# Kernel tuning notes

Hardware: AMD Instinct MI355X
Metric: run time of the kernel (lower is better)

## Reference

```python
import jax, jax.numpy as jnp
import numpy as np

D_MODEL = 512
H = 8
C = 2


def setup_inputs() -> dict:
    key = jax.random.key(0)
    kq, kk, kv = jax.random.split(key, 3)
    B, L = 16, 1024
    Q = jax.random.normal(kq, (B, L, D_MODEL), dtype=jnp.float32)
    K = jax.random.normal(kk, (B, L, D_MODEL), dtype=jnp.float32)
    V = jax.random.normal(kv, (B, L, D_MODEL), dtype=jnp.float32)
    return {"Q": Q, "K": K, "V": V}


def reference(Q, K, V):
    B, L, dm = Q.shape
    d = dm // H
    # [B, h, L, d]
    q = Q.reshape(B, L, H, d).transpose(0, 2, 1, 3)
    k = K.reshape(B, L, H, d).transpose(0, 2, 1, 3)
    v = V.reshape(B, L, H, d).transpose(0, 2, 1, 3)

    # auto-correlation via FFT along the time axis (axis=2)
    qf = jnp.fft.fft(q, axis=2)
    kf = jnp.fft.fft(k, axis=2)
    corr = jnp.fft.ifft(qf * jnp.conj(kf), axis=2).real.astype(Q.dtype)  # [B,h,L,d]

    topk = int(C * np.log(L))  # static
    # top-k over the lag axis (L); lax.top_k works on last axis
    w, idx = jax.lax.top_k(corr.transpose(0, 1, 3, 2), topk)  # [B,h,d,k]
    w = jax.nn.softmax(w, axis=-1)
    w = w.transpose(0, 1, 3, 2)      # [B,h,k,d]
    idx = idx.transpose(0, 1, 3, 2)  # [B,h,k,d]

    # time-delay aggregation: out[t] = sum_i w_i * v[min(idx_i + t, L-1)]
    t = jnp.arange(L)
    gidx = jnp.minimum(idx[:, :, :, None, :] + t[None, None, None, :, None], L - 1)  # [B,h,k,L,d]
    gathered = jnp.take_along_axis(v[:, :, None, :, :], gidx, axis=3)  # [B,h,k,L,d]
    out = jnp.einsum('bhkd,bhkld->bhld', w, gathered)  # [B,h,L,d]

    return out.transpose(0, 2, 1, 3).reshape(B, L, dm)
```

## Files before the change

kernel.cpp:

```cpp
#include <hip/hip_runtime.h>
#include <float.h>

#define LSEQ 1024
#define NCH  8192
#define TOPK 13

typedef short bf16x8 __attribute__((ext_vector_type(8)));
typedef float f32x16 __attribute__((ext_vector_type(16)));

#define CH_BYTES 12416

__device__ __forceinline__ unsigned swzA(unsigned a) {
  return a ^ ((a >> 3) & 48u) ^ ((a >> 1) & 32u);
}
__device__ __forceinline__ float resid(float x) {
  return x - __uint_as_float(__float_as_uint(x) & 0xffff0000u);
}
__device__ __forceinline__ f32x16 mfma_bf16(bf16x8 a, bf16x8 b, f32x16 c) {
  return __builtin_amdgcn_mfma_f32_32x32x16_bf16(a, b, c, 0, 0, 0);
}

__global__ __launch_bounds__(256) void corr_mega_kernel(const float* __restrict__ Qg,
                                                        const float* __restrict__ Kg,
                                                        const float* __restrict__ Vg,
                                                        float* __restrict__ outg) {
  __shared__ __align__(16) unsigned char lds_raw[4 * CH_BYTES];
  const int tid = threadIdx.x, wave = tid >> 6, lane = tid & 63;
  const int bid = blockIdx.x;
  const int cblk = (bid & 7) * 256 + (bid >> 3);
  const int cg0 = cblk * 4;
  const int b = cg0 >> 9, col0 = cg0 & 511;
  const int c = cg0 + wave;
  (void)c;
  unsigned char* myc = lds_raw + wave * CH_BYTES;

  {
    const float* Qb = Qg + ((size_t)b * 1024) * 512 + col0;
    const float* Kb = Kg + ((size_t)b * 1024) * 512 + col0;
#pragma unroll
    for (int j = 0; j < 4; ++j) {
      int t = tid + 256 * j;
      float4 kv = *(const float4*)(Kb + (size_t)t * 512);
      float4 qv = *(const float4*)(Qb + (size_t)t * 512);
      unsigned ka0 = swzA(4u * (unsigned)(t >> 1) + 2u * (unsigned)(t & 1));
      unsigned qa0 = 8u * (unsigned)(t >> 1) + 2u * (unsigned)(t & 1);
      float karr[4] = {kv.x, kv.y, kv.z, kv.w};
      float qarr[4] = {qv.x, qv.y, qv.z, qv.w};
#pragma unroll
      for (int cc = 0; cc < 4; ++cc) {
        unsigned char* ck = lds_raw + cc * CH_BYTES;
        unsigned khiv = __float_as_uint(karr[cc]) >> 16;
        unsigned klov = __float_as_uint(resid(karr[cc])) >> 16;
        *(unsigned short*)(ck + ka0)        = (unsigned short)khiv;
        *(unsigned short*)(ck + 2048 + ka0) = (unsigned short)klov;
        unsigned qhiv = __float_as_uint(qarr[cc]) >> 16;
        unsigned qlov = __float_as_uint(resid(qarr[cc])) >> 16;
        *(unsigned short*)(ck + 4096 + qa0)     = (unsigned short)qhiv;
        *(unsigned short*)(ck + 4096 + qa0 + 4) = (unsigned short)qlov;
        if (t < 8) {
          *(unsigned short*)(ck + 8192 + qa0)     = (unsigned short)qhiv;
          *(unsigned short*)(ck + 8192 + qa0 + 4) = (unsigned short)qlov;
        }
      }
    }
  }
  __syncthreads();

  {
    unsigned* qe = (unsigned*)(myc + 4096);
    unsigned* qo = (unsigned*)(myc + 8256);
    uint4 r0 = *(const uint4*)(qe + 16 * lane);
    uint4 r1 = *(const uint4*)(qe + 16 * lane + 4);
    uint4 r2 = *(const uint4*)(qe + 16 * lane + 8);
    uint4 r3 = *(const uint4*)(qe + 16 * lane + 12);
    uint2 r4 = *(const uint2*)(qe + 16 * lane + 16);
    unsigned h9[9] = {r0.x, r0.z, r1.x, r1.z, r2.x, r2.z, r3.x, r3.z, r4.x};
    unsigned l9[9] = {r0.y, r0.w, r1.y, r1.w, r2.y, r2.w, r3.y, r3.w, r4.y};
    unsigned o16[16];
#pragma unroll
    for (int i = 0; i < 8; ++i) {
      o16[2 * i]     = __builtin_amdgcn_alignbyte(h9[i + 1], h9[i], 2);
      o16[2 * i + 1] = __builtin_amdgcn_alignbyte(l9[i + 1], l9[i], 2);
    }
    *(uint4*)(qo + 16 * lane)      = make_uint4(o16[0],  o16[1],  o16[2],  o16[3]);
    *(uint4*)(qo + 16 * lane + 4)  = make_uint4(o16[4],  o16[5],  o16[6],  o16[7]);
    *(uint4*)(qo + 16 * lane + 8)  = make_uint4(o16[8],  o16[9],  o16[10], o16[11]);
    *(uint4*)(qo + 16 * lane + 12) = make_uint4(o16[12], o16[13], o16[14], o16[15]);
    if (lane == 0) {
      *(uint4*)(qo + 1024) = make_uint4(o16[0], o16[1], o16[2], o16[3]);
      *(uint4*)(qo + 1028) = make_uint4(o16[4], o16[5], o16[6], o16[7]);
    }
  }

  const int row = lane & 31, Hh = lane >> 5;
  const int rp  = 2 * (row & 15) + (row >> 4);
  unsigned e0   = (unsigned)((8 * Hh - rp) & 1023);
  const int par = rp & 1;
  const unsigned char* bArr = myc + (par ? 8256 : 4096);
  unsigned boff = (((par ? (e0 - 1) : e0) >> 1) * 8u);
  unsigned tb   = (unsigned)(64 * row + 16 * Hh);

  f32x16 d = {};
#pragma unroll 4
  for (int ks = 0; ks < 64; ++ks) {
    unsigned sa = swzA(tb);
    uint4 Ah = *(const uint4*)(myc + sa);
    uint4 Al = *(const uint4*)(myc + 2048 + sa);
    uint2 p0 = *(const uint2*)(bArr + boff);
    uint2 p1 = *(const uint2*)(bArr + boff + 8);
    uint2 p2 = *(const uint2*)(bArr + boff + 16);
    uint2 p3 = *(const uint2*)(bArr + boff + 24);
    bf16x8 fah = __builtin_bit_cast(bf16x8, Ah);
    bf16x8 fal = __builtin_bit_cast(bf16x8, Al);
    bf16x8 fbh = __builtin_bit_cast(bf16x8, make_uint4(p0.x, p1.x, p2.x, p3.x));
    bf16x8 fbl = __builtin_bit_cast(bf16x8, make_uint4(p0.y, p1.y, p2.y, p3.y));
    d = mfma_bf16(fah, fbh, d);
    d = mfma_bf16(fal, fbh, d);
    d = mfma_bf16(fah, fbl, d);
    tb   = (tb + 32u) & 2047u;
    boff = (boff + 64u) & 4095u;
  }

  float acc[16];
#pragma unroll
  for (int i = 0; i < 16; ++i) acc[i] = d[i];
  const int ibase = 128 * Hh + rp;

  float topv[TOPK]; int topi[TOPK];
  for (int r = 0; r < TOPK; ++r) {
    float m = -FLT_MAX; int mi = 0x7fffffff;
#pragma unroll
    for (int j = 0; j < 16; ++j) {
      int idx = ibase + 32 * ((j & 3) + 8 * (j >> 2));
      if (acc[j] > m || (acc[j] == m && idx < mi)) { m = acc[j]; mi = idx; }
    }
#pragma unroll
    for (int offx = 32; offx >= 1; offx >>= 1) {
      float om = __shfl_xor(m, offx);
      int   oi = __shfl_xor(mi, offx);
      if (om > m || (om == m && oi < mi)) { m = om; mi = oi; }
    }
    topv[r] = m; topi[r] = mi;
#pragma unroll
    for (int j = 0; j < 16; ++j)
      acc[j] = (ibase + 32 * ((j & 3) + 8 * (j >> 2)) == mi) ? -FLT_MAX : acc[j];
  }
  float mx = topv[0];
  float w[TOPK]; float wsum = 0.f;
#pragma unroll
  for (int r = 0; r < TOPK; ++r) { w[r] = __expf(topv[r] - mx); wsum += w[r]; }
  float inv = 1.0f / wsum;
  int di[TOPK];
#pragma unroll
  for (int r = 0; r < TOPK; ++r) { w[r] *= inv; di[r] = (1024 - topi[r]) & 1023; }

  __syncthreads();
  {
    const float* Vb = Vg + ((size_t)b * 1024) * 512 + col0;
#pragma unroll
    for (int j = 0; j < 4; ++j) {
      int t = tid + 256 * j;
      float4 vv = *(const float4*)(Vb + (size_t)t * 512);
      ((float*)(lds_raw + 0 * CH_BYTES))[t] = vv.x;
      ((float*)(lds_raw + 1 * CH_BYTES))[t] = vv.y;
      ((float*)(lds_raw + 2 * CH_BYTES))[t] = vv.z;
      ((float*)(lds_raw + 3 * CH_BYTES))[t] = vv.w;
    }
  }
  __syncthreads();

  {
    const float* vls = (const float*)myc;
    float* obuf = (float*)(myc + 8256);
#pragma unroll 4
    for (int j = 0; j < 16; ++j) {
      int t = lane + 64 * j;
      float a = 0.f;
#pragma unroll
      for (int i = 0; i < TOPK; ++i) {
        int src = di[i] + t; src = src < 1023 ? src : 1023;
        a += w[i] * vls[src];
      }
      obuf[t] = a;
    }
  }
  __syncthreads();

  {
    float* o = outg + ((size_t)b * 1024) * 512 + col0;
#pragma unroll
    for (int jj = 0; jj < 4; ++jj) {
      int t = tid + 256 * jj;
      float4 ov;
      ov.x = ((const float*)(lds_raw + 0 * CH_BYTES + 8256))[t];
      ov.y = ((const float*)(lds_raw + 1 * CH_BYTES + 8256))[t];
      ov.z = ((const float*)(lds_raw + 2 * CH_BYTES + 8256))[t];
      ov.w = ((const float*)(lds_raw + 3 * CH_BYTES + 8256))[t];
      *(float4*)(o + (size_t)t * 512) = ov;
    }
  }
}

extern "C" void kernel_launch(void* const* d_in, const int* in_sizes, int n_in,
                              void* d_out, int out_size, void* d_ws, size_t ws_size,
                              hipStream_t stream) {
  const float* Q = (const float*)d_in[0];
  const float* K = (const float*)d_in[1];
  const float* V = (const float*)d_in[2];
  float* out = (float*)d_out;
  (void)d_ws; (void)ws_size;

  corr_mega_kernel<<<NCH / 4, 256, 0, stream>>>(Q, K, V, out);
}
```

Baseline: 226.6 us.

## Drop shifted-Q LDS copy via alignbyte in MFMA loop, prefetch V into registers

Removes the precomputed odd-shifted Q buffer and instead builds the B fragments inside the MFMA loop with alignbyte from five 8-byte LDS reads. Per-wave LDS drops from 12416 to 8256 bytes, which allows more resident blocks per CU. V is also loaded into registers before the correlation GEMM, so its global latency overlaps the compute, and later written to LDS. The cost is extra ALU work and one more LDS read per iteration, plus 16 extra live registers across the MFMA and top-k phases.

```diff
diff --git a/kernel.cpp b/kernel.cpp
--- a/kernel.cpp
+++ b/kernel.cpp
@@ -8,7 +8,7 @@
 typedef short bf16x8 __attribute__((ext_vector_type(8)));
 typedef float f32x16 __attribute__((ext_vector_type(16)));
 
-#define CH_BYTES 12416
+#define CH_BYTES 8256
 
 __device__ __forceinline__ unsigned swzA(unsigned a) {
   return a ^ ((a >> 3) & 48u) ^ ((a >> 1) & 32u);
@@ -30,8 +30,6 @@
   const int cblk = (bid & 7) * 256 + (bid >> 3);
   const int cg0 = cblk * 4;
   const int b = cg0 >> 9, col0 = cg0 & 511;
-  const int c = cg0 + wave;
-  (void)c;
   unsigned char* myc = lds_raw + wave * CH_BYTES;
 
   {
@@ -66,38 +64,20 @@
   }
   __syncthreads();
 
+  float4 vreg[4];
   {
-    unsigned* qe = (unsigned*)(myc + 4096);
-    unsigned* qo = (unsigned*)(myc + 8256);
-    uint4 r0 = *(const uint4*)(qe + 16 * lane);
-    uint4 r1 = *(const uint4*)(qe + 16 * lane + 4);
-    uint4 r2 = *(const uint4*)(qe + 16 * lane + 8);
-    uint4 r3 = *(const uint4*)(qe + 16 * lane + 12);
-    uint2 r4 = *(const uint2*)(qe + 16 * lane + 16);
-    unsigned h9[9] = {r0.x, r0.z, r1.x, r1.z, r2.x, r2.z, r3.x, r3.z, r4.x};
-    unsigned l9[9] = {r0.y, r0.w, r1.y, r1.w, r2.y, r2.w, r3.y, r3.w, r4.y};
-    unsigned o16[16];
+    const float* Vb = Vg + ((size_t)b * 1024) * 512 + col0;
 #pragma unroll
-    for (int i = 0; i < 8; ++i) {
-      o16[2 * i]     = __builtin_amdgcn_alignbyte(h9[i + 1], h9[i], 2);
-      o16[2 * i + 1] = __builtin_amdgcn_alignbyte(l9[i + 1], l9[i], 2);
-    }
-    *(uint4*)(qo + 16 * lane)      = make_uint4(o16[0],  o16[1],  o16[2],  o16[3]);
-    *(uint4*)(qo + 16 * lane + 4)  = make_uint4(o16[4],  o16[5],  o16[6],  o16[7]);
-    *(uint4*)(qo + 16 * lane + 8)  = make_uint4(o16[8],  o16[9],  o16[10], o16[11]);
-    *(uint4*)(qo + 16 * lane + 12) = make_uint4(o16[12], o16[13], o16[14], o16[15]);
-    if (lane == 0) {
-      *(uint4*)(qo + 1024) = make_uint4(o16[0], o16[1], o16[2], o16[3]);
-      *(uint4*)(qo + 1028) = make_uint4(o16[4], o16[5], o16[6], o16[7]);
-    }
+    for (int j = 0; j < 4; ++j)
+      vreg[j] = *(const float4*)(Vb + (size_t)(tid + 256 * j) * 512);
   }
 
   const int row = lane & 31, Hh = lane >> 5;
   const int rp  = 2 * (row & 15) + (row >> 4);
   unsigned e0   = (unsigned)((8 * Hh - rp) & 1023);
-  const int par = rp & 1;
-  const unsigned char* bArr = myc + (par ? 8256 : 4096);
-  unsigned boff = (((par ? (e0 - 1) : e0) >> 1) * 8u);
+  const unsigned sh = 2u * (e0 & 1u);
+  const unsigned char* qeB = myc + 4096;
+  unsigned boff = (e0 >> 1) * 8u;
   unsigned tb   = (unsigned)(64 * row + 16 * Hh);
 
   f32x16 d = {};
@@ -106,14 +86,23 @@
     unsigned sa = swzA(tb);
     uint4 Ah = *(const uint4*)(myc + sa);
     uint4 Al = *(const uint4*)(myc + 2048 + sa);
-    uint2 p0 = *(const uint2*)(bArr + boff);
-    uint2 p1 = *(const uint2*)(bArr + boff + 8);
-    uint2 p2 = *(const uint2*)(bArr + boff + 16);
-    uint2 p3 = *(const uint2*)(bArr + boff + 24);
+    uint2 p0 = *(const uint2*)(qeB + boff);
+    uint2 p1 = *(const uint2*)(qeB + boff + 8);
+    uint2 p2 = *(const uint2*)(qeB + boff + 16);
+    uint2 p3 = *(const uint2*)(qeB + boff + 24);
+    uint2 p4 = *(const uint2*)(qeB + boff + 32);
+    unsigned bh0 = __builtin_amdgcn_alignbyte(p1.x, p0.x, sh);
+    unsigned bh1 = __builtin_amdgcn_alignbyte(p2.x, p1.x, sh);
+    unsigned bh2 = __builtin_amdgcn_alignbyte(p3.x, p2.x, sh);
+    unsigned bh3 = __builtin_amdgcn_alignbyte(p4.x, p3.x, sh);
+    unsigned bl0 = __builtin_amdgcn_alignbyte(p1.y, p0.y, sh);
+    unsigned bl1 = __builtin_amdgcn_alignbyte(p2.y, p1.y, sh);
+    unsigned bl2 = __builtin_amdgcn_alignbyte(p3.y, p2.y, sh);
+    unsigned bl3 = __builtin_amdgcn_alignbyte(p4.y, p3.y, sh);
     bf16x8 fah = __builtin_bit_cast(bf16x8, Ah);
     bf16x8 fal = __builtin_bit_cast(bf16x8, Al);
-    bf16x8 fbh = __builtin_bit_cast(bf16x8, make_uint4(p0.x, p1.x, p2.x, p3.x));
-    bf16x8 fbl = __builtin_bit_cast(bf16x8, make_uint4(p0.y, p1.y, p2.y, p3.y));
+    bf16x8 fbh = __builtin_bit_cast(bf16x8, make_uint4(bh0, bh1, bh2, bh3));
+    bf16x8 fbl = __builtin_bit_cast(bf16x8, make_uint4(bl0, bl1, bl2, bl3));
     d = mfma_bf16(fah, fbh, d);
     d = mfma_bf16(fal, fbh, d);
     d = mfma_bf16(fah, fbl, d);
@@ -155,23 +144,19 @@
   for (int r = 0; r < TOPK; ++r) { w[r] *= inv; di[r] = (1024 - topi[r]) & 1023; }
 
   __syncthreads();
-  {
-    const float* Vb = Vg + ((size_t)b * 1024) * 512 + col0;
 #pragma unroll
-    for (int j = 0; j < 4; ++j) {
-      int t = tid + 256 * j;
-      float4 vv = *(const float4*)(Vb + (size_t)t * 512);
-      ((float*)(lds_raw + 0 * CH_BYTES))[t] = vv.x;
-      ((float*)(lds_raw + 1 * CH_BYTES))[t] = vv.y;
-      ((float*)(lds_raw + 2 * CH_BYTES))[t] = vv.z;
-      ((float*)(lds_raw + 3 * CH_BYTES))[t] = vv.w;
-    }
+  for (int j = 0; j < 4; ++j) {
+    int t = tid + 256 * j;
+    ((float*)(lds_raw + 0 * CH_BYTES))[t] = vreg[j].x;
+    ((float*)(lds_raw + 1 * CH_BYTES))[t] = vreg[j].y;
+    ((float*)(lds_raw + 2 * CH_BYTES))[t] = vreg[j].z;
+    ((float*)(lds_raw + 3 * CH_BYTES))[t] = vreg[j].w;
   }
   __syncthreads();
 
   {
     const float* vls = (const float*)myc;
-    float* obuf = (float*)(myc + 8256);
+    float* obuf = (float*)(myc + 4096);
 #pragma unroll 4
     for (int j = 0; j < 16; ++j) {
       int t = lane + 64 * j;
@@ -192,10 +177,10 @@
     for (int jj = 0; jj < 4; ++jj) {
       int t = tid + 256 * jj;
       float4 ov;
-      ov.x = ((const float*)(lds_raw + 0 * CH_BYTES + 8256))[t];
-      ov.y = ((const float*)(lds_raw + 1 * CH_BYTES + 8256))[t];
-      ov.z = ((const float*)(lds_raw + 2 * CH_BYTES + 8256))[t];
-      ov.w = ((const float*)(lds_raw + 3 * CH_BYTES + 8256))[t];
+      ov.x = ((const float*)(lds_raw + 0 * CH_BYTES + 4096))[t];
+      ov.y = ((const float*)(lds_raw + 1 * CH_BYTES + 4096))[t];
+      ov.z = ((const float*)(lds_raw + 2 * CH_BYTES + 4096))[t];
+      ov.w = ((const float*)(lds_raw + 3 * CH_BYTES + 4096))[t];
       *(float4*)(o + (size_t)t * 512) = ov;
     }
   }
```

Measured after the change: 212.8 us. -6.1%, faster.
